# Optimization experiments

Hardware: AMD Instinct MI355X
Metric: run time of the kernel (lower is better)

Reference implementation:

```python
import jax, jax.numpy as jnp
import numpy as np

NUM_HEADS = 16
DK = 64
DV = 64
MASK_FILL = -10000000000.0


def setup_inputs() -> dict:
    key = jax.random.key(0)
    kq, kk, kv, km = jax.random.split(key, 4)
    B, L, D = 2, 2048, NUM_HEADS * DK
    Q = jax.random.normal(kq, (B, L, D), dtype=jnp.float32)
    K = jax.random.normal(kk, (B, L, D), dtype=jnp.float32)
    V = jax.random.normal(kv, (B, L, NUM_HEADS * DV), dtype=jnp.float32)
    mask = jax.random.randint(km, (B, L, L), 0, 2).astype(jnp.bool_)
    return {"Q": Q, "K": K, "V": V, "mask": mask}


def reference(Q, K, V, mask):
    B, Lq, _ = Q.shape
    Lk = K.shape[1]
    # split heads: [B, H, L, d]
    q = Q.reshape(B, Lq, NUM_HEADS, DK).transpose(0, 2, 1, 3)
    k = K.reshape(B, Lk, NUM_HEADS, DK).transpose(0, 2, 1, 3)
    v = V.reshape(B, Lk, NUM_HEADS, DV).transpose(0, 2, 1, 3)
    # scores [B, H, Lq, Lk]; NOTE: original masks BEFORE scaling by 1/sqrt(dk)
    scores = jnp.einsum("bhqd,bhkd->bhqk", q, k)
    scores = jnp.where(mask[:, None, :, :], MASK_FILL, scores)
    scores = scores / jnp.sqrt(jnp.asarray(DK, dtype=scores.dtype))
    attn = jax.nn.softmax(scores, axis=-1)
    out = jnp.einsum("bhqk,bhkd->bhqd", attn, v)  # [B, H, Lq, dv]
    # concat heads back: [B, Lq, H*dv]
    return out.transpose(0, 2, 1, 3).reshape(B, Lq, NUM_HEADS * DV)
```

## Files before the change

### kernel.cpp

```cpp
#include <hip/hip_runtime.h>
#include <hip/hip_bf16.h>

#define NH 16
#define DH 64
#define LL 2048
#define DM 1024
#define SCALE2 0.1803368801111204f
#define GUARD_HI 60.0f
#define NT2 (LL / 128)

typedef __attribute__((ext_vector_type(4))) float f32x4;
typedef __attribute__((ext_vector_type(16))) float f32x16;
typedef __attribute__((ext_vector_type(8))) short bf16x8;

__device__ __forceinline__ unsigned pk2(float lo, float hi) {
    __hip_bfloat162 h = __float22bfloat162_rn(make_float2(lo, hi));
    union { __hip_bfloat162 h; unsigned u; } c; c.h = h; return c.u;
}
__device__ __forceinline__ bf16x8 cvt8(float4 a, float4 b) {
    union { bf16x8 v; unsigned u[4]; } r;
    r.u[0] = pk2(a.x, a.y); r.u[1] = pk2(a.z, a.w);
    r.u[2] = pk2(b.x, b.y); r.u[3] = pk2(b.z, b.w);
    return r.v;
}
__device__ __forceinline__ float exp2_fast(float x) {
    float y;
    asm("v_exp_f32 %0, %1" : "=v"(y) : "v"(x));
    return y;
}
__device__ __forceinline__ float keepf(float p, unsigned nw, int idx) {
    int k = (int)(nw << (31 - idx)) >> 31;
    unsigned pu = __builtin_bit_cast(unsigned, p) & (unsigned)k;
    return __builtin_bit_cast(float, pu);
}

__global__ __launch_bounds__(256) void pack_mask4(const void* __restrict__ mask,
                                                  unsigned* __restrict__ bits)
{
    const int tid = threadIdx.x;
    const int lane = tid & 63;
    const int* mw = (const int*)mask;
    unsigned long long bad = __ballot((unsigned)mw[lane] > 1u);
    const bool is_int = (bad == 0ULL);

    const int wid = blockIdx.x * 256 + tid;
    const int kb = wid & 3;
    const int q = (wid >> 2) & 2047;
    const int t = (wid >> 13) & 15;
    const int b = wid >> 17;
    unsigned m = 0;
    if (is_int) {
        const int* p = (const int*)mask + ((size_t)b * 2048 + q) * 2048
                     + t * 128 + kb * 32;
        #pragma unroll
        for (int h = 0; h < 2; ++h)
            #pragma unroll
            for (int blk = 0; blk < 4; ++blk) {
                int4 v = *(const int4*)(p + 8 * blk + 4 * h);
                int base = 8 * blk + 4 * h;
                m |= (v.x ? 1u : 0u) << base;
                m |= (v.y ? 1u : 0u) << (base + 1);
                m |= (v.z ? 1u : 0u) << (base + 2);
                m |= (v.w ? 1u : 0u) << (base + 3);
            }
    } else {
        const unsigned char* pb = (const unsigned char*)mask
                                + ((size_t)b * 2048 + q) * 2048 + t * 128 + kb * 32;
        #pragma unroll
        for (int h = 0; h < 2; ++h)
            #pragma unroll
            for (int blk = 0; blk < 4; ++blk) {
                unsigned v = *(const unsigned*)(pb + 8 * blk + 4 * h);
                int base = 8 * blk + 4 * h;
                m |= (v & 1u) << base;
                m |= ((v >> 8) & 1u) << (base + 1);
                m |= ((v >> 16) & 1u) << (base + 2);
                m |= ((v >> 24) & 1u) << (base + 3);
            }
    }
    bits[wid] = ~m;
}

__global__ __launch_bounds__(256) void prep_k(const float* __restrict__ K,
                                              short* __restrict__ Kb)
{
    const int kt = blockIdx.x, h = blockIdx.y, b = blockIdx.z;
    const int tid = threadIdx.x;
    const int key = tid >> 2;
    const int c8 = (tid & 3) * 2;
    const float* src = K + ((size_t)b * LL + kt * 64 + key) * DM + h * DH + c8 * 8;
    float4 a = *(const float4*)(src);
    float4 bb = *(const float4*)(src + 4);
    float4 c = *(const float4*)(src + 8);
    float4 d = *(const float4*)(src + 12);
    short* dst = Kb + (((size_t)(b * NH + h) * 32 + kt) << 12);
    *(bf16x8*)&dst[key * 64 + ((c8 ^ (key & 7)) << 3)] = cvt8(a, bb);
    *(bf16x8*)&dst[key * 64 + (((c8 + 1) ^ (key & 7)) << 3)] = cvt8(c, d);
}

__global__ __launch_bounds__(256) void prep_v(const float* __restrict__ V,
                                              short* __restrict__ Vb)
{
    const int kt = blockIdx.x, h = blockIdx.y, b = blockIdx.z;
    const int tid = threadIdx.x;
    const int kp = tid & 31;
    const int dv8 = tid >> 5;
    const float* s0 = V + ((size_t)b * LL + kt * 64 + 2 * kp) * DM + h * DH + dv8 * 8;
    float4 a0 = *(const float4*)(s0);
    float4 a1 = *(const float4*)(s0 + 4);
    float4 b0 = *(const float4*)(s0 + DM);
    float4 b1 = *(const float4*)(s0 + DM + 4);
    float av[8] = {a0.x, a0.y, a0.z, a0.w, a1.x, a1.y, a1.z, a1.w};
    float bv[8] = {b0.x, b0.y, b0.z, b0.w, b1.x, b1.y, b1.z, b1.w};
    short* dst = Vb + (((size_t)(b * NH + h) * 32 + kt) << 12);
    const int w16 = (2 * kp) & 15;
    const int kg = kp >> 3;
    const int half = (w16 >> 2) & 1;
    const int i0 = (w16 & 3) + 4 * (w16 >> 3);
    const int sg = kg * 2 + half;
    #pragma unroll
    for (int j = 0; j < 8; ++j) {
        int dv = dv8 * 8 + j;
        int off = dv * 64 + ((sg ^ (dv & 7)) << 3) + i0;
        *(unsigned*)&dst[off] = pk2(av[j], bv[j]);
    }
}

__global__ __launch_bounds__(256, 2) void mha_fwd3(
    const float* __restrict__ Q, const short* __restrict__ Kb,
    const short* __restrict__ Vb, const unsigned* __restrict__ mbits,
    float* __restrict__ out)
{
    const int bid = blockIdx.x;
    const int xcd = bid & 7;
    const int j = bid >> 3;
    const int pair = xcd * 4 + (j >> 4);
    const int qblk = j & 15;
    const int hd = pair & 15;
    const int b = pair >> 4;

    const int tid = threadIdx.x;
    const int w = tid >> 6;
    const int lane = tid & 63;
    const int lq = lane & 31;
    const int hh = lane >> 5;

    const int qbase = qblk * 128 + w * 32;

    __shared__ short Kt[2][2][4096];
    __shared__ short Vt[2][2][4096];

    const short* Ktile0 = Kb + ((size_t)(b * NH + hd) << 17);
    const short* Vtile0 = Vb + ((size_t)(b * NH + hd) << 17);
    const unsigned* Mp = mbits + (size_t)b * (16 * 8192) + (qbase + lq) * 4;

    uint4 mreg = *(const uint4*)(Mp);
    #pragma unroll
    for (int sub = 0; sub < 2; ++sub)
        #pragma unroll
        for (int i = 0; i < 2; ++i) {
            __builtin_amdgcn_global_load_lds(
                (const unsigned*)(Ktile0 + sub * 4096 + w * 1024 + i * 512 + lane * 8),
                (unsigned*)&Kt[0][sub][w * 1024 + i * 512 + lane * 8], 16, 0, 0);
            __builtin_amdgcn_global_load_lds(
                (const unsigned*)(Vtile0 + sub * 4096 + w * 1024 + i * 512 + lane * 8),
                (unsigned*)&Vt[0][sub][w * 1024 + i * 512 + lane * 8], 16, 0, 0);
        }

    bf16x8 qf[4];
    {
        const float* qp = Q + ((size_t)b * LL + qbase + lq) * DM + hd * DH + 8 * hh;
        #pragma unroll
        for (int d16 = 0; d16 < 4; ++d16) {
            float4 a = *(const float4*)(qp + 16 * d16);
            float4 c = *(const float4*)(qp + 16 * d16 + 4);
            a.x *= SCALE2; a.y *= SCALE2; a.z *= SCALE2; a.w *= SCALE2;
            c.x *= SCALE2; c.y *= SCALE2; c.z *= SCALE2; c.w *= SCALE2;
            qf[d16] = cvt8(a, c);
        }
    }

    f32x16 o0, o1;
    #pragma unroll
    for (int i = 0; i < 16; ++i) { o0[i] = 0.f; o1[i] = 0.f; }
    float l_own = 0.f;
    float m_shift = 0.f;
    const int sh4 = 4 * hh;

    asm volatile("s_waitcnt vmcnt(0)" ::: "memory");
    __builtin_amdgcn_s_barrier();

    #pragma unroll 2
    for (int t = 0; t < NT2; ++t) {
        const int cur = t & 1;
        const uint4 m4 = mreg;
        if (t + 1 < NT2) {
            mreg = *(const uint4*)(Mp + (size_t)(t + 1) * 8192);
            const short* kb_ = Ktile0 + (size_t)(t + 1) * 8192;
            const short* vb_ = Vtile0 + (size_t)(t + 1) * 8192;
            #pragma unroll
            for (int sub = 0; sub < 2; ++sub)
                #pragma unroll
                for (int i = 0; i < 2; ++i) {
                    __builtin_amdgcn_global_load_lds(
                        (const unsigned*)(kb_ + sub * 4096 + w * 1024 + i * 512 + lane * 8),
                        (unsigned*)&Kt[cur ^ 1][sub][w * 1024 + i * 512 + lane * 8], 16, 0, 0);
                    __builtin_amdgcn_global_load_lds(
                        (const unsigned*)(vb_ + sub * 4096 + w * 1024 + i * 512 + lane * 8),
                        (unsigned*)&Vt[cur ^ 1][sub][w * 1024 + i * 512 + lane * 8], 16, 0, 0);
                }
            asm volatile("s_waitcnt vmcnt(9)" ::: "memory");
        } else {
            asm volatile("s_waitcnt vmcnt(0)" ::: "memory");
        }
        __builtin_amdgcn_s_barrier();
        __builtin_amdgcn_sched_barrier(0);

        f32x16 s[4];
        __builtin_amdgcn_s_setprio(1);
        #pragma unroll
        for (int kb2 = 0; kb2 < 4; ++kb2) {
            const int sub = kb2 >> 1;
            const int keyrow = (kb2 & 1) * 32 + lq;
            const int swz = keyrow & 7;
            f32x16 acc;
            #pragma unroll
            for (int i = 0; i < 16; ++i) acc[i] = 0.f;
            #pragma unroll
            for (int d16 = 0; d16 < 4; ++d16) {
                bf16x8 kf = *(const bf16x8*)
                    &Kt[cur][sub][keyrow * 64 + (((2 * d16 + hh) ^ swz) << 3)];
                acc = __builtin_amdgcn_mfma_f32_32x32x16_bf16(kf, qf[d16], acc, 0, 0, 0);
            }
            s[kb2] = acc;
        }
        __builtin_amdgcn_s_setprio(0);

        float mx = -1e30f;
        #pragma unroll
        for (int kb2 = 0; kb2 < 4; ++kb2) {
            float a0 = fmaxf(fmaxf(s[kb2][0], s[kb2][1]), fmaxf(s[kb2][2], s[kb2][3]));
            float a1 = fmaxf(fmaxf(s[kb2][4], s[kb2][5]), fmaxf(s[kb2][6], s[kb2][7]));
            float a2 = fmaxf(fmaxf(s[kb2][8], s[kb2][9]), fmaxf(s[kb2][10], s[kb2][11]));
            float a3 = fmaxf(fmaxf(s[kb2][12], s[kb2][13]), fmaxf(s[kb2][14], s[kb2][15]));
            mx = fmaxf(mx, fmaxf(fmaxf(a0, a1), fmaxf(a2, a3)));
        }
        if (__builtin_expect(m_shift != 0.0f, 0)) {
            #pragma unroll
            for (int kb2 = 0; kb2 < 4; ++kb2)
                #pragma unroll
                for (int r = 0; r < 16; ++r) s[kb2][r] -= m_shift;
            mx -= m_shift;
        }
        if (!__all(mx <= GUARD_HI)) {
            float tmax = fmaxf(mx, __shfl_xor(mx, 32, 64));
            float shift = tmax - 30.0f;
            m_shift += shift;
            float alpha = exp2_fast(-shift);
            #pragma unroll
            for (int i = 0; i < 16; ++i) { o0[i] *= alpha; o1[i] *= alpha; }
            l_own *= alpha;
            #pragma unroll
            for (int kb2 = 0; kb2 < 4; ++kb2)
                #pragma unroll
                for (int r = 0; r < 16; ++r) s[kb2][r] -= shift;
        }

        unsigned nws0 = m4.x >> sh4, nws1 = m4.y >> sh4;
        unsigned nws2 = m4.z >> sh4, nws3 = m4.w >> sh4;
        unsigned nws[4] = {nws0, nws1, nws2, nws3};
        bf16x8 pfr[4][2];
        float lsum = 0.f;
        #pragma unroll
        for (int kb2 = 0; kb2 < 4; ++kb2) {
            float p[16];
            #pragma unroll
            for (int r = 0; r < 16; ++r)
                p[r] = keepf(exp2_fast(s[kb2][r]), nws[kb2], 8 * (r >> 2) + (r & 3));
            float q1[8];
            #pragma unroll
            for (int i = 0; i < 8; ++i) q1[i] = p[2 * i] + p[2 * i + 1];
            lsum += ((q1[0] + q1[1]) + (q1[2] + q1[3]))
                  + ((q1[4] + q1[5]) + (q1[6] + q1[7]));
            union { bf16x8 v; unsigned u[4]; } pa, pb;
            pa.u[0] = pk2(p[0], p[1]);  pa.u[1] = pk2(p[2], p[3]);
            pa.u[2] = pk2(p[4], p[5]);  pa.u[3] = pk2(p[6], p[7]);
            pb.u[0] = pk2(p[8], p[9]);  pb.u[1] = pk2(p[10], p[11]);
            pb.u[2] = pk2(p[12], p[13]); pb.u[3] = pk2(p[14], p[15]);
            pfr[kb2][0] = pa.v;
            pfr[kb2][1] = pb.v;
        }
        l_own += lsum;

        __builtin_amdgcn_s_setprio(1);
        #pragma unroll
        for (int kb2 = 0; kb2 < 4; ++kb2) {
            const int sub = kb2 >> 1;
            #pragma unroll
            for (int kkb = 0; kkb < 2; ++kkb) {
                const int m = (kb2 & 1) * 2 + kkb;
                const int slot = ((2 * m + hh) ^ (lq & 7)) << 3;
                bf16x8 v0 = *(const bf16x8*)&Vt[cur][sub][lq * 64 + slot];
                bf16x8 v1 = *(const bf16x8*)&Vt[cur][sub][(32 + lq) * 64 + slot];
                o0 = __builtin_amdgcn_mfma_f32_32x32x16_bf16(v0, pfr[kb2][kkb], o0, 0, 0, 0);
                o1 = __builtin_amdgcn_mfma_f32_32x32x16_bf16(v1, pfr[kb2][kkb], o1, 0, 0, 0);
            }
        }
        __builtin_amdgcn_s_setprio(0);

        __builtin_amdgcn_sched_barrier(0);
        __builtin_amdgcn_s_barrier();
    }

    float l = l_own + __shfl_xor(l_own, 32, 64);
    float inv = __builtin_amdgcn_rcpf(l);
    float* fout = out + ((size_t)b * LL + qbase + lq) * DM + hd * DH + 4 * hh;
    #pragma unroll
    for (int rg = 0; rg < 4; ++rg) {
        float4 v0, v1;
        v0.x = o0[4 * rg + 0] * inv; v0.y = o0[4 * rg + 1] * inv;
        v0.z = o0[4 * rg + 2] * inv; v0.w = o0[4 * rg + 3] * inv;
        v1.x = o1[4 * rg + 0] * inv; v1.y = o1[4 * rg + 1] * inv;
        v1.z = o1[4 * rg + 2] * inv; v1.w = o1[4 * rg + 3] * inv;
        *(float4*)(fout + 8 * rg) = v0;
        *(float4*)(fout + 32 + 8 * rg) = v1;
    }
}

extern "C" void kernel_launch(void* const* d_in, const int* in_sizes, int n_in,
                              void* d_out, int out_size, void* d_ws, size_t ws_size,
                              hipStream_t stream) {
    const float* Q = (const float*)d_in[0];
    const float* K = (const float*)d_in[1];
    const float* V = (const float*)d_in[2];
    const void* mask = d_in[3];
    float* out = (float*)d_out;

    unsigned* bits = (unsigned*)d_ws;
    const size_t MASK_B = (size_t)2 * 16 * 2048 * 4 * 4;
    const size_t KV_B = (size_t)2 * NH * 32 * 4096 * 2;
    short* Kb = (short*)((char*)d_ws + MASK_B);
    short* Vb = (short*)((char*)d_ws + MASK_B + KV_B);

    pack_mask4<<<dim3(2 * 16 * 2048 * 4 / 256), dim3(256), 0, stream>>>(mask, bits);
    prep_k<<<dim3(32, NH, 2), dim3(256), 0, stream>>>(K, Kb);
    prep_v<<<dim3(32, NH, 2), dim3(256), 0, stream>>>(V, Vb);
    mha_fwd3<<<dim3(512), dim3(256), 0, stream>>>(Q, Kb, Vb, bits, out);
}
```

Measured before the change: 82.60 us.

## Split key range across two wave groups per block and merge partial softmax

The attention kernel now runs 512 threads per block, with two groups of four waves. Each group processes half of the key sequence in 64-key tiles, and the groups' partial outputs and row sums are combined through LDS at the end. The K/V prep layouts drop the XOR swizzle in favour of a d16-major contiguous layout, and the mask packing becomes row-major. The goal is more waves in flight and a shorter serial loop per wave, at the cost of an extra LDS reduction, possible LDS bank conflicts from the unswizzled layout, and higher register pressure under launch_bounds(512,4).

```diff
diff --git a/kernel.cpp b/kernel.cpp
--- a/kernel.cpp
+++ b/kernel.cpp
@@ -7,7 +7,7 @@
 #define DM 1024
 #define SCALE2 0.1803368801111204f
 #define GUARD_HI 60.0f
-#define NT2 (LL / 128)
+#define NT64 16
 
 typedef __attribute__((ext_vector_type(4))) float f32x4;
 typedef __attribute__((ext_vector_type(16))) float f32x16;
@@ -34,8 +34,8 @@
     return __builtin_bit_cast(float, pu);
 }
 
-__global__ __launch_bounds__(256) void pack_mask4(const void* __restrict__ mask,
-                                                  unsigned* __restrict__ bits)
+__global__ __launch_bounds__(256) void pack_mask(const void* __restrict__ mask,
+                                                 unsigned* __restrict__ bits)
 {
     const int tid = threadIdx.x;
     const int lane = tid & 63;
@@ -44,39 +44,30 @@
     const bool is_int = (bad == 0ULL);
 
     const int wid = blockIdx.x * 256 + tid;
-    const int kb = wid & 3;
-    const int q = (wid >> 2) & 2047;
-    const int t = (wid >> 13) & 15;
-    const int b = wid >> 17;
+    const int kw = wid & 63;
+    const int q64 = wid >> 6;
     unsigned m = 0;
     if (is_int) {
-        const int* p = (const int*)mask + ((size_t)b * 2048 + q) * 2048
-                     + t * 128 + kb * 32;
-        #pragma unroll
-        for (int h = 0; h < 2; ++h)
-            #pragma unroll
-            for (int blk = 0; blk < 4; ++blk) {
-                int4 v = *(const int4*)(p + 8 * blk + 4 * h);
-                int base = 8 * blk + 4 * h;
-                m |= (v.x ? 1u : 0u) << base;
-                m |= (v.y ? 1u : 0u) << (base + 1);
-                m |= (v.z ? 1u : 0u) << (base + 2);
-                m |= (v.w ? 1u : 0u) << (base + 3);
-            }
+        const int* p = (const int*)mask + (size_t)q64 * LL + kw * 32;
+        #pragma unroll
+        for (int j = 0; j < 32; j += 4) {
+            int4 v = *(const int4*)(p + j);
+            m |= (v.x ? 1u : 0u) << j;
+            m |= (v.y ? 1u : 0u) << (j + 1);
+            m |= (v.z ? 1u : 0u) << (j + 2);
+            m |= (v.w ? 1u : 0u) << (j + 3);
+        }
     } else {
-        const unsigned char* pb = (const unsigned char*)mask
-                                + ((size_t)b * 2048 + q) * 2048 + t * 128 + kb * 32;
-        #pragma unroll
-        for (int h = 0; h < 2; ++h)
-            #pragma unroll
-            for (int blk = 0; blk < 4; ++blk) {
-                unsigned v = *(const unsigned*)(pb + 8 * blk + 4 * h);
-                int base = 8 * blk + 4 * h;
-                m |= (v & 1u) << base;
-                m |= ((v >> 8) & 1u) << (base + 1);
-                m |= ((v >> 16) & 1u) << (base + 2);
-                m |= ((v >> 24) & 1u) << (base + 3);
-            }
+        const unsigned* p = (const unsigned*)((const unsigned char*)mask
+                                              + (size_t)q64 * LL + kw * 32);
+        #pragma unroll
+        for (int j = 0; j < 8; ++j) {
+            unsigned v = p[j];
+            m |= (v & 1u) << (4 * j);
+            m |= ((v >> 8) & 1u) << (4 * j + 1);
+            m |= ((v >> 16) & 1u) << (4 * j + 2);
+            m |= ((v >> 24) & 1u) << (4 * j + 3);
+        }
     }
     bits[wid] = ~m;
 }
@@ -87,15 +78,15 @@
     const int kt = blockIdx.x, h = blockIdx.y, b = blockIdx.z;
     const int tid = threadIdx.x;
     const int key = tid >> 2;
-    const int c8 = (tid & 3) * 2;
-    const float* src = K + ((size_t)b * LL + kt * 64 + key) * DM + h * DH + c8 * 8;
-    float4 a = *(const float4*)(src);
-    float4 bb = *(const float4*)(src + 4);
-    float4 c = *(const float4*)(src + 8);
-    float4 d = *(const float4*)(src + 12);
+    const int d16 = tid & 3;
+    const float* src = K + ((size_t)b * LL + kt * 64 + key) * DM + h * DH + d16 * 16;
+    float4 f0 = *(const float4*)(src);
+    float4 f1 = *(const float4*)(src + 4);
+    float4 f2 = *(const float4*)(src + 8);
+    float4 f3 = *(const float4*)(src + 12);
     short* dst = Kb + (((size_t)(b * NH + h) * 32 + kt) << 12);
-    *(bf16x8*)&dst[key * 64 + ((c8 ^ (key & 7)) << 3)] = cvt8(a, bb);
-    *(bf16x8*)&dst[key * 64 + (((c8 + 1) ^ (key & 7)) << 3)] = cvt8(c, d);
+    *(bf16x8*)&dst[d16 * 1024 + key * 16] = cvt8(f0, f1);
+    *(bf16x8*)&dst[d16 * 1024 + key * 16 + 8] = cvt8(f2, f3);
 }
 
 __global__ __launch_bounds__(256) void prep_v(const float* __restrict__ V,
@@ -113,20 +104,19 @@
     float av[8] = {a0.x, a0.y, a0.z, a0.w, a1.x, a1.y, a1.z, a1.w};
     float bv[8] = {b0.x, b0.y, b0.z, b0.w, b1.x, b1.y, b1.z, b1.w};
     short* dst = Vb + (((size_t)(b * NH + h) * 32 + kt) << 12);
-    const int w16 = (2 * kp) & 15;
-    const int kg = kp >> 3;
-    const int half = (w16 >> 2) & 1;
+    const int key0 = 2 * kp;
+    const int m = key0 >> 4;
+    const int w16 = key0 & 15;
+    const int hh = (w16 >> 2) & 1;
     const int i0 = (w16 & 3) + 4 * (w16 >> 3);
-    const int sg = kg * 2 + half;
     #pragma unroll
     for (int j = 0; j < 8; ++j) {
         int dv = dv8 * 8 + j;
-        int off = dv * 64 + ((sg ^ (dv & 7)) << 3) + i0;
-        *(unsigned*)&dst[off] = pk2(av[j], bv[j]);
-    }
-}
-
-__global__ __launch_bounds__(256, 2) void mha_fwd3(
+        *(unsigned*)&dst[m * 1024 + dv * 16 + hh * 8 + i0] = pk2(av[j], bv[j]);
+    }
+}
+
+__global__ __launch_bounds__(512, 4) void mha_fwd4(
     const float* __restrict__ Q, const short* __restrict__ Kb,
     const short* __restrict__ Vb, const unsigned* __restrict__ mbits,
     float* __restrict__ out)
@@ -141,31 +131,36 @@
 
     const int tid = threadIdx.x;
     const int w = tid >> 6;
+    const int g = w >> 2;
+    const int wg = w & 3;
     const int lane = tid & 63;
     const int lq = lane & 31;
     const int hh = lane >> 5;
 
-    const int qbase = qblk * 128 + w * 32;
-
-    __shared__ short Kt[2][2][4096];
-    __shared__ short Vt[2][2][4096];
+    const int qbase = qblk * 128 + wg * 32;
+
+    __shared__ short smem[32768];
+    #define KOFF(gg, cc) (((gg) * 2 + (cc)) * 4096)
+    #define VOFF(gg, cc) (16384 + ((gg) * 2 + (cc)) * 4096)
 
     const short* Ktile0 = Kb + ((size_t)(b * NH + hd) << 17);
     const short* Vtile0 = Vb + ((size_t)(b * NH + hd) << 17);
-    const unsigned* Mp = mbits + (size_t)b * (16 * 8192) + (qbase + lq) * 4;
-
-    uint4 mreg = *(const uint4*)(Mp);
-    #pragma unroll
-    for (int sub = 0; sub < 2; ++sub)
-        #pragma unroll
-        for (int i = 0; i < 2; ++i) {
+    const unsigned* Mrow = mbits + ((size_t)b * LL + qbase + lq) * 64 + g * 32;
+
+    uint2 mreg = *(const uint2*)(Mrow);
+    {
+        const short* kb_ = Ktile0 + (size_t)(g * 16) * 4096;
+        const short* vb_ = Vtile0 + (size_t)(g * 16) * 4096;
+        #pragma unroll
+        for (int c = 0; c < 2; ++c) {
             __builtin_amdgcn_global_load_lds(
-                (const unsigned*)(Ktile0 + sub * 4096 + w * 1024 + i * 512 + lane * 8),
-                (unsigned*)&Kt[0][sub][w * 1024 + i * 512 + lane * 8], 16, 0, 0);
+                (const unsigned*)(kb_ + wg * 1024 + c * 512 + lane * 8),
+                (unsigned*)&smem[KOFF(g, 0) + wg * 1024 + c * 512], 16, 0, 0);
             __builtin_amdgcn_global_load_lds(
-                (const unsigned*)(Vtile0 + sub * 4096 + w * 1024 + i * 512 + lane * 8),
-                (unsigned*)&Vt[0][sub][w * 1024 + i * 512 + lane * 8], 16, 0, 0);
-        }
+                (const unsigned*)(vb_ + wg * 1024 + c * 512 + lane * 8),
+                (unsigned*)&smem[VOFF(g, 0) + wg * 1024 + c * 512], 16, 0, 0);
+        }
+    }
 
     bf16x8 qf[4];
     {
@@ -191,45 +186,40 @@
     __builtin_amdgcn_s_barrier();
 
     #pragma unroll 2
-    for (int t = 0; t < NT2; ++t) {
+    for (int t = 0; t < NT64; ++t) {
         const int cur = t & 1;
-        const uint4 m4 = mreg;
-        if (t + 1 < NT2) {
-            mreg = *(const uint4*)(Mp + (size_t)(t + 1) * 8192);
-            const short* kb_ = Ktile0 + (size_t)(t + 1) * 8192;
-            const short* vb_ = Vtile0 + (size_t)(t + 1) * 8192;
-            #pragma unroll
-            for (int sub = 0; sub < 2; ++sub)
-                #pragma unroll
-                for (int i = 0; i < 2; ++i) {
-                    __builtin_amdgcn_global_load_lds(
-                        (const unsigned*)(kb_ + sub * 4096 + w * 1024 + i * 512 + lane * 8),
-                        (unsigned*)&Kt[cur ^ 1][sub][w * 1024 + i * 512 + lane * 8], 16, 0, 0);
-                    __builtin_amdgcn_global_load_lds(
-                        (const unsigned*)(vb_ + sub * 4096 + w * 1024 + i * 512 + lane * 8),
-                        (unsigned*)&Vt[cur ^ 1][sub][w * 1024 + i * 512 + lane * 8], 16, 0, 0);
-                }
-            asm volatile("s_waitcnt vmcnt(9)" ::: "memory");
+        const uint2 m2 = mreg;
+        if (t + 1 < NT64) {
+            mreg = *(const uint2*)(Mrow + 2 * (t + 1));
+            const short* kb_ = Ktile0 + (size_t)(g * 16 + t + 1) * 4096;
+            const short* vb_ = Vtile0 + (size_t)(g * 16 + t + 1) * 4096;
+            #pragma unroll
+            for (int c = 0; c < 2; ++c) {
+                __builtin_amdgcn_global_load_lds(
+                    (const unsigned*)(kb_ + wg * 1024 + c * 512 + lane * 8),
+                    (unsigned*)&smem[KOFF(g, cur ^ 1) + wg * 1024 + c * 512], 16, 0, 0);
+                __builtin_amdgcn_global_load_lds(
+                    (const unsigned*)(vb_ + wg * 1024 + c * 512 + lane * 8),
+                    (unsigned*)&smem[VOFF(g, cur ^ 1) + wg * 1024 + c * 512], 16, 0, 0);
+            }
+            asm volatile("s_waitcnt vmcnt(5)" ::: "memory");
         } else {
             asm volatile("s_waitcnt vmcnt(0)" ::: "memory");
         }
         __builtin_amdgcn_s_barrier();
         __builtin_amdgcn_sched_barrier(0);
 
-        f32x16 s[4];
+        f32x16 s[2];
         __builtin_amdgcn_s_setprio(1);
         #pragma unroll
-        for (int kb2 = 0; kb2 < 4; ++kb2) {
-            const int sub = kb2 >> 1;
-            const int keyrow = (kb2 & 1) * 32 + lq;
-            const int swz = keyrow & 7;
+        for (int kb2 = 0; kb2 < 2; ++kb2) {
             f32x16 acc;
             #pragma unroll
             for (int i = 0; i < 16; ++i) acc[i] = 0.f;
             #pragma unroll
             for (int d16 = 0; d16 < 4; ++d16) {
                 bf16x8 kf = *(const bf16x8*)
-                    &Kt[cur][sub][keyrow * 64 + (((2 * d16 + hh) ^ swz) << 3)];
+                    &smem[KOFF(g, cur) + d16 * 1024 + kb2 * 512 + lq * 16 + hh * 8];
                 acc = __builtin_amdgcn_mfma_f32_32x32x16_bf16(kf, qf[d16], acc, 0, 0, 0);
             }
             s[kb2] = acc;
@@ -238,7 +228,7 @@
 
         float mx = -1e30f;
         #pragma unroll
-        for (int kb2 = 0; kb2 < 4; ++kb2) {
+        for (int kb2 = 0; kb2 < 2; ++kb2) {
             float a0 = fmaxf(fmaxf(s[kb2][0], s[kb2][1]), fmaxf(s[kb2][2], s[kb2][3]));
             float a1 = fmaxf(fmaxf(s[kb2][4], s[kb2][5]), fmaxf(s[kb2][6], s[kb2][7]));
             float a2 = fmaxf(fmaxf(s[kb2][8], s[kb2][9]), fmaxf(s[kb2][10], s[kb2][11]));
@@ -247,7 +237,7 @@
         }
         if (__builtin_expect(m_shift != 0.0f, 0)) {
             #pragma unroll
-            for (int kb2 = 0; kb2 < 4; ++kb2)
+            for (int kb2 = 0; kb2 < 2; ++kb2)
                 #pragma unroll
                 for (int r = 0; r < 16; ++r) s[kb2][r] -= m_shift;
             mx -= m_shift;
@@ -261,18 +251,16 @@
             for (int i = 0; i < 16; ++i) { o0[i] *= alpha; o1[i] *= alpha; }
             l_own *= alpha;
             #pragma unroll
-            for (int kb2 = 0; kb2 < 4; ++kb2)
+            for (int kb2 = 0; kb2 < 2; ++kb2)
                 #pragma unroll
                 for (int r = 0; r < 16; ++r) s[kb2][r] -= shift;
         }
 
-        unsigned nws0 = m4.x >> sh4, nws1 = m4.y >> sh4;
-        unsigned nws2 = m4.z >> sh4, nws3 = m4.w >> sh4;
-        unsigned nws[4] = {nws0, nws1, nws2, nws3};
-        bf16x8 pfr[4][2];
+        const unsigned nws[2] = {m2.x >> sh4, m2.y >> sh4};
+        bf16x8 pfr[2][2];
         float lsum = 0.f;
         #pragma unroll
-        for (int kb2 = 0; kb2 < 4; ++kb2) {
+        for (int kb2 = 0; kb2 < 2; ++kb2) {
             float p[16];
             #pragma unroll
             for (int r = 0; r < 16; ++r)
@@ -283,9 +271,9 @@
             lsum += ((q1[0] + q1[1]) + (q1[2] + q1[3]))
                   + ((q1[4] + q1[5]) + (q1[6] + q1[7]));
             union { bf16x8 v; unsigned u[4]; } pa, pb;
-            pa.u[0] = pk2(p[0], p[1]);  pa.u[1] = pk2(p[2], p[3]);
-            pa.u[2] = pk2(p[4], p[5]);  pa.u[3] = pk2(p[6], p[7]);
-            pb.u[0] = pk2(p[8], p[9]);  pb.u[1] = pk2(p[10], p[11]);
+            pa.u[0] = pk2(p[0], p[1]);   pa.u[1] = pk2(p[2], p[3]);
+            pa.u[2] = pk2(p[4], p[5]);   pa.u[3] = pk2(p[6], p[7]);
+            pb.u[0] = pk2(p[8], p[9]);   pb.u[1] = pk2(p[10], p[11]);
             pb.u[2] = pk2(p[12], p[13]); pb.u[3] = pk2(p[14], p[15]);
             pfr[kb2][0] = pa.v;
             pfr[kb2][1] = pb.v;
@@ -294,17 +282,14 @@
 
         __builtin_amdgcn_s_setprio(1);
         #pragma unroll
-        for (int kb2 = 0; kb2 < 4; ++kb2) {
-            const int sub = kb2 >> 1;
-            #pragma unroll
-            for (int kkb = 0; kkb < 2; ++kkb) {
-                const int m = (kb2 & 1) * 2 + kkb;
-                const int slot = ((2 * m + hh) ^ (lq & 7)) << 3;
-                bf16x8 v0 = *(const bf16x8*)&Vt[cur][sub][lq * 64 + slot];
-                bf16x8 v1 = *(const bf16x8*)&Vt[cur][sub][(32 + lq) * 64 + slot];
-                o0 = __builtin_amdgcn_mfma_f32_32x32x16_bf16(v0, pfr[kb2][kkb], o0, 0, 0, 0);
-                o1 = __builtin_amdgcn_mfma_f32_32x32x16_bf16(v1, pfr[kb2][kkb], o1, 0, 0, 0);
-            }
+        for (int m = 0; m < 4; ++m) {
+            bf16x8 pf = pfr[m >> 1][m & 1];
+            bf16x8 v0 = *(const bf16x8*)
+                &smem[VOFF(g, cur) + m * 1024 + lq * 16 + hh * 8];
+            bf16x8 v1 = *(const bf16x8*)
+                &smem[VOFF(g, cur) + m * 1024 + (32 + lq) * 16 + hh * 8];
+            o0 = __builtin_amdgcn_mfma_f32_32x32x16_bf16(v0, pf, o0, 0, 0, 0);
+            o1 = __builtin_amdgcn_mfma_f32_32x32x16_bf16(v1, pf, o1, 0, 0, 0);
         }
         __builtin_amdgcn_s_setprio(0);
 
@@ -312,19 +297,43 @@
         __builtin_amdgcn_s_barrier();
     }
 
-    float l = l_own + __shfl_xor(l_own, 32, 64);
-    float inv = __builtin_amdgcn_rcpf(l);
-    float* fout = out + ((size_t)b * LL + qbase + lq) * DM + hd * DH + 4 * hh;
-    #pragma unroll
-    for (int rg = 0; rg < 4; ++rg) {
-        float4 v0, v1;
-        v0.x = o0[4 * rg + 0] * inv; v0.y = o0[4 * rg + 1] * inv;
-        v0.z = o0[4 * rg + 2] * inv; v0.w = o0[4 * rg + 3] * inv;
-        v1.x = o1[4 * rg + 0] * inv; v1.y = o1[4 * rg + 1] * inv;
-        v1.z = o1[4 * rg + 2] * inv; v1.w = o1[4 * rg + 3] * inv;
-        *(float4*)(fout + 8 * rg) = v0;
-        *(float4*)(fout + 32 + 8 * rg) = v1;
-    }
+    float* cb = (float*)smem;
+    const int cbase = (wg * 64 + lane) * 34;
+    if (g == 1) {
+        #pragma unroll
+        for (int i = 0; i < 16; ++i) { cb[cbase + i] = o0[i]; cb[cbase + 16 + i] = o1[i]; }
+        cb[cbase + 32] = l_own;
+        cb[cbase + 33] = m_shift;
+    }
+    __syncthreads();
+    if (g == 0) {
+        float msB = cb[cbase + 33];
+        float lB = cb[cbase + 32];
+        float M = fmaxf(m_shift, msB);
+        float aA = exp2_fast(m_shift - M);
+        float aB = exp2_fast(msB - M);
+        float lc = l_own * aA + lB * aB;
+        lc += __shfl_xor(lc, 32, 64);
+        float inv = __builtin_amdgcn_rcpf(lc);
+        #pragma unroll
+        for (int i = 0; i < 16; ++i) {
+            o0[i] = (o0[i] * aA + cb[cbase + i] * aB) * inv;
+            o1[i] = (o1[i] * aA + cb[cbase + 16 + i] * aB) * inv;
+        }
+        float* fout = out + ((size_t)b * LL + qbase + lq) * DM + hd * DH + 4 * hh;
+        #pragma unroll
+        for (int rg = 0; rg < 4; ++rg) {
+            float4 v0, v1;
+            v0.x = o0[4 * rg + 0]; v0.y = o0[4 * rg + 1];
+            v0.z = o0[4 * rg + 2]; v0.w = o0[4 * rg + 3];
+            v1.x = o1[4 * rg + 0]; v1.y = o1[4 * rg + 1];
+            v1.z = o1[4 * rg + 2]; v1.w = o1[4 * rg + 3];
+            *(float4*)(fout + 8 * rg) = v0;
+            *(float4*)(fout + 32 + 8 * rg) = v1;
+        }
+    }
+    #undef KOFF
+    #undef VOFF
 }
 
 extern "C" void kernel_launch(void* const* d_in, const int* in_sizes, int n_in,
@@ -337,13 +346,13 @@
     float* out = (float*)d_out;
 
     unsigned* bits = (unsigned*)d_ws;
-    const size_t MASK_B = (size_t)2 * 16 * 2048 * 4 * 4;
+    const size_t MASK_B = (size_t)2 * LL * 64 * 4;
     const size_t KV_B = (size_t)2 * NH * 32 * 4096 * 2;
     short* Kb = (short*)((char*)d_ws + MASK_B);
     short* Vb = (short*)((char*)d_ws + MASK_B + KV_B);
 
-    pack_mask4<<<dim3(2 * 16 * 2048 * 4 / 256), dim3(256), 0, stream>>>(mask, bits);
+    pack_mask<<<dim3(2 * LL * 64 / 256), dim3(256), 0, stream>>>(mask, bits);
     prep_k<<<dim3(32, NH, 2), dim3(256), 0, stream>>>(K, Kb);
     prep_v<<<dim3(32, NH, 2), dim3(256), 0, stream>>>(V, Vb);
-    mha_fwd3<<<dim3(512), dim3(256), 0, stream>>>(Q, Kb, Vb, bits, out);
-}
+    mha_fwd4<<<dim3(512), dim3(512), 0, stream>>>(Q, Kb, Vb, bits, out);
+}
```

After: 97.74 us. 18.3% more time.
